# Performance work log

Measured on AMD Instinct MI355X. Metric: run time of the kernel, lower is better.

The kernel has to match this reference:

```python
import jax, jax.numpy as jnp
import numpy as np

UP = 4  # upsample factor of DispUpsampleBySlantedPlane


def _l1_warp_cost(fea_l, fea_r, disp):
    """Warp fea_r horizontally by disp (grid_sample bilinear, zeros padding,
    align_corners=True) and return per-pixel L1 distance over channels.
    fea_l, fea_r: [B, C, H, W]; disp: [B, H, W] -> returns [B, H, W]."""
    B, C, H, W = fea_l.shape
    x = jnp.arange(W, dtype=disp.dtype)
    xf = x[None, None, :] - disp              # sample position in right image
    x0 = jnp.floor(xf)
    w1 = xf - x0                              # weight for x0+1
    w0 = 1.0 - w1
    x0i = x0.astype(jnp.int32)
    x1i = x0i + 1
    v0 = ((x0i >= 0) & (x0i < W)).astype(fea_l.dtype)  # zeros padding masks
    v1 = ((x1i >= 0) & (x1i < W)).astype(fea_l.dtype)
    x0c = jnp.clip(x0i, 0, W - 1)
    x1c = jnp.clip(x1i, 0, W - 1)
    idx0 = jnp.broadcast_to(x0c[:, None, :, :], (B, C, H, W))
    idx1 = jnp.broadcast_to(x1c[:, None, :, :], (B, C, H, W))
    g0 = jnp.take_along_axis(fea_r, idx0, axis=3)
    g1 = jnp.take_along_axis(fea_r, idx1, axis=3)
    warped = g0 * (w0 * v0)[:, None] + g1 * (w1 * v1)[:, None]
    return jnp.sum(jnp.abs(fea_l - warped), axis=1)  # L1 over channels


def _tile_warping(tile_plane, fea_l, fea_r):
    B, C, H, W = fea_l.shape
    h, w = tile_plane.shape[2], tile_plane.shape[3]
    d = tile_plane[:, 0]   # [B, h, w]
    dx = tile_plane[:, 1]
    dy = tile_plane[:, 2]
    # slanted-plane offsets for the 4x4 sub-pixels, centered at (UP-1)/2 = 1.5
    off = jnp.arange(UP, dtype=fea_l.dtype) - (UP - 1) / 2.0
    outs = []
    for disp_d in (-1.0, 0.0, 1.0):
        # disp0[b, di, dj, th, tw] = (d + disp_d) + off[di]*dy + off[dj]*dx
        disp0 = ((d + disp_d)[:, None, None]
                 + off[None, :, None, None, None] * dy[:, None, None]
                 + off[None, None, :, None, None] * dx[:, None, None])
        # PixelShuffle(4): full-res disparity [B, H, W]
        disp_full = disp0.transpose(0, 3, 1, 4, 2).reshape(B, H, W)
        cv = _l1_warp_cost(fea_l, fea_r, disp_full)        # [B, H, W]
        # cv[:, :, i::4, j::4] for i,j in 0..3, concatenated on channel dim
        local = cv.reshape(B, h, UP, w, UP).transpose(0, 2, 4, 1, 3)
        outs.append(local.reshape(B, UP * UP, h, w))       # [B, 16, h, w]
    return jnp.concatenate(outs, axis=1)                   # [B, 48, h, w]


def setup_inputs() -> dict:
    key = jax.random.key(0)
    k1, k2, k3 = jax.random.split(key, 3)
    B, C, H, W = 4, 16, 512, 960
    h, w = H // UP, W // UP
    tile_plane = jax.random.normal(k1, (B, 3, h, w), dtype=jnp.float32)
    fea_l = jax.random.normal(k2, (B, C, H, W), dtype=jnp.float32)
    fea_r = jax.random.normal(k3, (B, C, H, W), dtype=jnp.float32)
    return {"tile_plane": tile_plane, "fea_l": fea_l, "fea_r": fea_r}


def reference(tile_plane, fea_l, fea_r):
    return _tile_warping(tile_plane, fea_l, fea_r)
```

## Files before the change

### kernel.cpp

```cpp
#include <hip/hip_runtime.h>


#define NB 4
#define NC 16
#define NH 512
#define NW 960
#define TH 128
#define TW 240
#define HW (NH * NW)
#define GUARD 16
#define CHUNK 8
#define CBUF (2 * GUARD + CHUNK * NW)

typedef const __attribute__((address_space(1))) unsigned int* gas_u32;
typedef __attribute__((address_space(3))) unsigned int* las_u32;

__device__ __forceinline__ void stage16(const float* g, float* l) {
    __builtin_amdgcn_global_load_lds((gas_u32)g, (las_u32)l, 16, 0, 0);
}

__global__ __launch_bounds__(960, 8) void tile_warp_kernel(
    const float* __restrict__ tp,
    const float* __restrict__ fl,
    const float* __restrict__ fr,
    float* __restrict__ out)
{
    const int u = threadIdx.x;
    const int Y = blockIdx.x;
    const int b = blockIdx.y;
    const int y = Y >> 2, i = Y & 3;
    const int T = u >> 2, j = u & 3;

    __shared__ float smem[2][CBUF];

    const float* frrow = fr + (size_t)(b * NC) * HW + (size_t)Y * NW;
    const float* flrow = fl + (size_t)(b * NC) * HW + (size_t)Y * NW + u;

    {
        const int s0 = u, s1 = u + 960;
        stage16(frrow + (s0 / 240) * HW + 4 * (s0 % 240), &smem[0][GUARD + 4 * s0]);
        stage16(frrow + (s1 / 240) * HW + 4 * (s1 % 240), &smem[0][GUARD + 4 * s1]);
    }

    const int tpb = (b * 3 * TH + y) * TW + T;
    const float d   = tp[tpb];
    const float dxv = tp[tpb + TH * TW];
    const float dyv = tp[tpb + 2 * TH * TW];
    const float base = d + ((float)i - 1.5f) * dyv + ((float)j - 1.5f) * dxv;
    const float xf  = (float)u - base;
    const float x0f = floorf(xf);
    const float w1  = xf - x0f;
    const float w0  = 1.0f - w1;
    const int   x0  = (int)x0f;
    const int   p   = x0 - 1;
    const int   p_cl = max(min(p, NW + 12), -GUARD);

    float w0k[3], w1k[3];
#pragma unroll
    for (int kk = 0; kk < 3; ++kk) {
        const int xa = p + 2 - kk;
        const int xb = p + 3 - kk;
        w0k[kk] = (xa >= 0 && xa < NW) ? w0 : 0.0f;
        w1k[kk] = (xb >= 0 && xb < NW) ? w1 : 0.0f;
    }
    float acc0 = 0.f, acc1 = 0.f, acc2 = 0.f;

    __syncthreads();

    {
        const float* frrow1 = frrow + CHUNK * HW;
        const int s0 = u, s1 = u + 960;
        stage16(frrow1 + (s0 / 240) * HW + 4 * (s0 % 240), &smem[1][GUARD + 4 * s0]);
        stage16(frrow1 + (s1 / 240) * HW + 4 * (s1 % 240), &smem[1][GUARD + 4 * s1]);
    }

    {
        float flv[CHUNK];
#pragma unroll
        for (int c = 0; c < CHUNK; ++c) flv[c] = flrow[c * HW];
#pragma unroll
        for (int c = 0; c < CHUNK; ++c) {
            const float* L = &smem[0][GUARD + c * NW + p_cl];
            const float m0 = L[0], m1 = L[1], m2 = L[2], m3 = L[3];
            const float wv0 = m2 * w0k[0] + m3 * w1k[0];
            const float wv1 = m1 * w0k[1] + m2 * w1k[1];
            const float wv2 = m0 * w0k[2] + m1 * w1k[2];
            acc0 += fabsf(flv[c] - wv0);
            acc1 += fabsf(flv[c] - wv1);
            acc2 += fabsf(flv[c] - wv2);
        }
    }

    __syncthreads();

    {
        float flv[CHUNK];
#pragma unroll
        for (int c = 0; c < CHUNK; ++c) flv[c] = flrow[(CHUNK + c) * HW];
#pragma unroll
        for (int c = 0; c < CHUNK; ++c) {
            const float* L = &smem[1][GUARD + c * NW + p_cl];
            const float m0 = L[0], m1 = L[1], m2 = L[2], m3 = L[3];
            const float wv0 = m2 * w0k[0] + m3 * w1k[0];
            const float wv1 = m1 * w0k[1] + m2 * w1k[1];
            const float wv2 = m0 * w0k[2] + m1 * w1k[2];
            acc0 += fabsf(flv[c] - wv0);
            acc1 += fabsf(flv[c] - wv1);
            acc2 += fabsf(flv[c] - wv2);
        }
    }

    const size_t obase = ((size_t)(b * 48 + i * 4 + j) * TH + y) * TW + T;
    out[obase]                        = acc0;
    out[obase + 16 * (size_t)TH * TW] = acc1;
    out[obase + 32 * (size_t)TH * TW] = acc2;
}

extern "C" void kernel_launch(void* const* d_in, const int* in_sizes, int n_in,
                              void* d_out, int out_size, void* d_ws, size_t ws_size,
                              hipStream_t stream) {
    const float* tp = (const float*)d_in[0];
    const float* fl = (const float*)d_in[1];
    const float* fr = (const float*)d_in[2];
    float* out = (float*)d_out;

    dim3 grid(NH, NB);
    dim3 block(960);
    tile_warp_kernel<<<grid, block, 0, stream>>>(tp, fl, fr, out);
}
```

Before: 272.6 us.

## Replace LDS staging with direct clamped global gathers and smaller blocks

Removes the double-buffered global-to-LDS staging of the right-feature row and its barriers. Each thread now gathers its four neighbouring samples straight from global memory using clamped indices, relying on the cache for reuse. Blocks shrink from 960 to 320 threads over a 3D grid to raise scheduling flexibility. The risk is more global/cache traffic from uncoalesced gathers and the loss of explicit data reuse through LDS.

```diff
diff --git a/kernel.cpp b/kernel.cpp
--- a/kernel.cpp
+++ b/kernel.cpp
@@ -8,39 +8,21 @@
 #define TH 128
 #define TW 240
 #define HW (NH * NW)
-#define GUARD 16
-#define CHUNK 8
-#define CBUF (2 * GUARD + CHUNK * NW)
 
-typedef const __attribute__((address_space(1))) unsigned int* gas_u32;
-typedef __attribute__((address_space(3))) unsigned int* las_u32;
-
-__device__ __forceinline__ void stage16(const float* g, float* l) {
-    __builtin_amdgcn_global_load_lds((gas_u32)g, (las_u32)l, 16, 0, 0);
-}
-
-__global__ __launch_bounds__(960, 8) void tile_warp_kernel(
+__global__ __launch_bounds__(320, 8) void tile_warp_kernel(
     const float* __restrict__ tp,
     const float* __restrict__ fl,
     const float* __restrict__ fr,
     float* __restrict__ out)
 {
-    const int u = threadIdx.x;
-    const int Y = blockIdx.x;
-    const int b = blockIdx.y;
+    const int u = blockIdx.x * 320 + threadIdx.x;
+    const int Y = blockIdx.y;
+    const int b = blockIdx.z;
     const int y = Y >> 2, i = Y & 3;
     const int T = u >> 2, j = u & 3;
 
-    __shared__ float smem[2][CBUF];
-
     const float* frrow = fr + (size_t)(b * NC) * HW + (size_t)Y * NW;
     const float* flrow = fl + (size_t)(b * NC) * HW + (size_t)Y * NW + u;
-
-    {
-        const int s0 = u, s1 = u + 960;
-        stage16(frrow + (s0 / 240) * HW + 4 * (s0 % 240), &smem[0][GUARD + 4 * s0]);
-        stage16(frrow + (s1 / 240) * HW + 4 * (s1 % 240), &smem[0][GUARD + 4 * s1]);
-    }
 
     const int tpb = (b * 3 * TH + y) * TW + T;
     const float d   = tp[tpb];
@@ -53,7 +35,6 @@
     const float w0  = 1.0f - w1;
     const int   x0  = (int)x0f;
     const int   p   = x0 - 1;
-    const int   p_cl = max(min(p, NW + 12), -GUARD);
 
     float w0k[3], w1k[3];
 #pragma unroll
@@ -63,51 +44,28 @@
         w0k[kk] = (xa >= 0 && xa < NW) ? w0 : 0.0f;
         w1k[kk] = (xb >= 0 && xb < NW) ? w1 : 0.0f;
     }
+
+    const int i0 = min(max(p    , 0), NW - 1);
+    const int i1 = min(max(p + 1, 0), NW - 1);
+    const int i2 = min(max(p + 2, 0), NW - 1);
+    const int i3 = min(max(p + 3, 0), NW - 1);
+
     float acc0 = 0.f, acc1 = 0.f, acc2 = 0.f;
 
-    __syncthreads();
-
-    {
-        const float* frrow1 = frrow + CHUNK * HW;
-        const int s0 = u, s1 = u + 960;
-        stage16(frrow1 + (s0 / 240) * HW + 4 * (s0 % 240), &smem[1][GUARD + 4 * s0]);
-        stage16(frrow1 + (s1 / 240) * HW + 4 * (s1 % 240), &smem[1][GUARD + 4 * s1]);
-    }
-
-    {
-        float flv[CHUNK];
 #pragma unroll
-        for (int c = 0; c < CHUNK; ++c) flv[c] = flrow[c * HW];
-#pragma unroll
-        for (int c = 0; c < CHUNK; ++c) {
-            const float* L = &smem[0][GUARD + c * NW + p_cl];
-            const float m0 = L[0], m1 = L[1], m2 = L[2], m3 = L[3];
-            const float wv0 = m2 * w0k[0] + m3 * w1k[0];
-            const float wv1 = m1 * w0k[1] + m2 * w1k[1];
-            const float wv2 = m0 * w0k[2] + m1 * w1k[2];
-            acc0 += fabsf(flv[c] - wv0);
-            acc1 += fabsf(flv[c] - wv1);
-            acc2 += fabsf(flv[c] - wv2);
-        }
-    }
-
-    __syncthreads();
-
-    {
-        float flv[CHUNK];
-#pragma unroll
-        for (int c = 0; c < CHUNK; ++c) flv[c] = flrow[(CHUNK + c) * HW];
-#pragma unroll
-        for (int c = 0; c < CHUNK; ++c) {
-            const float* L = &smem[1][GUARD + c * NW + p_cl];
-            const float m0 = L[0], m1 = L[1], m2 = L[2], m3 = L[3];
-            const float wv0 = m2 * w0k[0] + m3 * w1k[0];
-            const float wv1 = m1 * w0k[1] + m2 * w1k[1];
-            const float wv2 = m0 * w0k[2] + m1 * w1k[2];
-            acc0 += fabsf(flv[c] - wv0);
-            acc1 += fabsf(flv[c] - wv1);
-            acc2 += fabsf(flv[c] - wv2);
-        }
+    for (int c = 0; c < NC; ++c) {
+        const float* frc = frrow + (size_t)c * HW;
+        const float m0  = frc[i0];
+        const float m1  = frc[i1];
+        const float m2  = frc[i2];
+        const float m3  = frc[i3];
+        const float flv = flrow[(size_t)c * HW];
+        const float wv0 = m2 * w0k[0] + m3 * w1k[0];
+        const float wv1 = m1 * w0k[1] + m2 * w1k[1];
+        const float wv2 = m0 * w0k[2] + m1 * w1k[2];
+        acc0 += fabsf(flv - wv0);
+        acc1 += fabsf(flv - wv1);
+        acc2 += fabsf(flv - wv2);
     }
 
     const size_t obase = ((size_t)(b * 48 + i * 4 + j) * TH + y) * TW + T;
@@ -124,7 +82,7 @@
     const float* fr = (const float*)d_in[2];
     float* out = (float*)d_out;
 
-    dim3 grid(NH, NB);
-    dim3 block(960);
+    dim3 grid(3, NH, NB);
+    dim3 block(320);
     tile_warp_kernel<<<grid, block, 0, stream>>>(tp, fl, fr, out);
 }
```

Measured after the change: 301.8 us. +10.7%, slower.
